# Performance work log

Hardware: AMD Instinct MI355X
Metric: run time of the kernel (lower is better)

Reference implementation:

```python
import jax, jax.numpy as jnp
import numpy as np

COMMITMENT_COST = 0.25
NUM_EMBEDDINGS = 1024
EMBEDDING_DIM = 512  # win_size(8) * num_pellets(64)


def setup_inputs() -> dict:
    key = jax.random.key(0)
    k1, k2 = jax.random.split(key)
    inputs = jax.random.normal(k1, (64, 256, EMBEDDING_DIM), dtype=jnp.float32)
    # matches torch init: uniform_(-1/K, 1/K)
    lim = 1.0 / NUM_EMBEDDINGS
    emb_weight = jax.random.uniform(k2, (NUM_EMBEDDINGS, EMBEDDING_DIM),
                                    dtype=jnp.float32, minval=-lim, maxval=lim)
    return {"inputs": inputs, "emb_weight": emb_weight}


def reference(inputs, emb_weight):
    batch_size = inputs.shape[0]
    input_shape = inputs.shape
    flat = inputs.reshape(-1, EMBEDDING_DIM)  # [N, D]

    distances = (jnp.sum(flat * flat, axis=1, keepdims=True)
                 + jnp.sum(emb_weight * emb_weight, axis=1)
                 - 2.0 * flat @ emb_weight.T)
    encoding_indices = jnp.argmin(distances, axis=1)  # [N]

    # gather instead of one-hot matmul (same math)
    quantized = emb_weight[encoding_indices].reshape(input_shape)

    e_latent_loss = jnp.mean((jax.lax.stop_gradient(quantized) - inputs) ** 2)
    q_latent_loss = jnp.mean((quantized - jax.lax.stop_gradient(inputs)) ** 2)
    loss_vq = q_latent_loss + COMMITMENT_COST * e_latent_loss

    # straight-through estimator
    quantized = inputs + jax.lax.stop_gradient(quantized - inputs)

    encoding_indices = encoding_indices.reshape(batch_size, -1)
    return loss_vq, quantized, encoding_indices
```

## Files before the change

kernel.cpp:

```cpp
#include <hip/hip_runtime.h>
#include <cfloat>

#define NROWS  16384
#define DIM    512
#define KC     1024
#define QELEMS (NROWS * DIM)

#define NSPLIT 8

typedef float  floatx4 __attribute__((ext_vector_type(4)));
typedef _Float16 half8 __attribute__((ext_vector_type(8)));
typedef _Float16 half4 __attribute__((ext_vector_type(4)));

__device__ __forceinline__ void gl_lds16(const _Float16* g, void* l) {
    __builtin_amdgcn_global_load_lds(
        (const __attribute__((address_space(1))) unsigned int*)g,
        (__attribute__((address_space(3))) unsigned int*)l,
        16, 0, 0);
}

__global__ __launch_bounds__(256) void prep_a_kernel(const float* __restrict__ A,
                                                     float* __restrict__ xsq,
                                                     _Float16* __restrict__ ah,
                                                     _Float16* __restrict__ al,
                                                     unsigned long long* __restrict__ packed,
                                                     float* __restrict__ out) {
    if (blockIdx.x == 0 && threadIdx.x == 0) out[0] = 0.f;
    int wave = threadIdx.x >> 6, lane = threadIdx.x & 63;
    int row = blockIdx.x * 4 + wave;
    const float4* Mr = (const float4*)(A + (size_t)row * DIM);
    float4 va = Mr[lane];
    float4 vb = Mr[lane + 64];
    float s = 0.f;
    s += va.x*va.x + va.y*va.y + va.z*va.z + va.w*va.w;
    s += vb.x*vb.x + vb.y*vb.y + vb.z*vb.z + vb.w*vb.w;
    #pragma unroll
    for (int off = 32; off; off >>= 1) s += __shfl_down(s, off, 64);
    if (lane == 0) { xsq[row] = s; packed[row] = ~0ULL; }

    float xa[4] = {va.x, va.y, va.z, va.w}, xb[4] = {vb.x, vb.y, vb.z, vb.w};
    half4 ha, la, hb, lb;
    #pragma unroll
    for (int e = 0; e < 4; ++e) {
        float t = xa[e] * 2048.0f;
        _Float16 h = (_Float16)t;
        ha[e] = h; la[e] = (_Float16)(t - (float)h);
        t = xb[e] * 2048.0f;
        h = (_Float16)t;
        hb[e] = h; lb[e] = (_Float16)(t - (float)h);
    }
    _Float16* ar = ah + (size_t)row * DIM;
    _Float16* lr = al + (size_t)row * DIM;
    ((half4*)ar)[lane]      = ha;
    ((half4*)lr)[lane]      = la;
    ((half4*)ar)[lane + 64] = hb;
    ((half4*)lr)[lane + 64] = lb;
}

__global__ __launch_bounds__(256) void prep_e_kernel(const float* __restrict__ E,
                                                     float* __restrict__ esq,
                                                     _Float16* __restrict__ eh,
                                                     _Float16* __restrict__ el) {
    int wave = threadIdx.x >> 6, lane = threadIdx.x & 63;
    int row = blockIdx.x * 4 + wave;
    const float4* Mr = (const float4*)(E + (size_t)row * DIM);
    float4 va = Mr[lane];
    float4 vb = Mr[lane + 64];
    float s = 0.f;
    s += va.x*va.x + va.y*va.y + va.z*va.z + va.w*va.w;
    s += vb.x*vb.x + vb.y*vb.y + vb.z*vb.z + vb.w*vb.w;
    #pragma unroll
    for (int off = 32; off; off >>= 1) s += __shfl_down(s, off, 64);
    if (lane == 0) esq[row] = s;

    float xa[4] = {va.x, va.y, va.z, va.w}, xb[4] = {vb.x, vb.y, vb.z, vb.w};
    half4 ha, la, hb, lb;
    #pragma unroll
    for (int e = 0; e < 4; ++e) {
        float t = xa[e] * 65536.0f;
        _Float16 h = (_Float16)t;
        ha[e] = h; la[e] = (_Float16)(t - (float)h);
        t = xb[e] * 65536.0f;
        h = (_Float16)t;
        hb[e] = h; lb[e] = (_Float16)(t - (float)h);
    }
    _Float16* hr = eh + (size_t)row * DIM;
    _Float16* lr = el + (size_t)row * DIM;
    ((half4*)hr)[lane]      = ha;
    ((half4*)lr)[lane]      = la;
    ((half4*)hr)[lane + 64] = hb;
    ((half4*)lr)[lane + 64] = lb;
}

__global__ __launch_bounds__(256) void mfma_argmin_kernel(const _Float16* __restrict__ ah,
                                                          const _Float16* __restrict__ al,
                                                          const _Float16* __restrict__ eh,
                                                          const _Float16* __restrict__ el,
                                                          const float* __restrict__ esq,
                                                          const float* __restrict__ xsq,
                                                          unsigned long long* __restrict__ packed) {
    __shared__ half8 AhT[512], AlT[512], EhT[512], ElT[512];
    __shared__ float redv[128][2];
    __shared__ int   redi[128][2];

    const int tid = threadIdx.x;
    const int lane = tid & 63, wave = tid >> 6;
    const int wm = wave >> 1, wn = wave & 1;
    const int tx = lane & 15, qd = lane >> 4;
    const int bm = blockIdx.x & 127, bn = blockIdx.x >> 7;
    const int m0 = bm * 128, c0 = bn * 128;

    const int rowL = (wave & 1) * 64 + lane;
    const int kqL  = wave >> 1;
    size_t offA = (size_t)(m0 + rowL) * DIM + kqL * 8;
    size_t offE = (size_t)(c0 + rowL) * DIM + kqL * 8;
    const int cb0 = wave * 64, cb1 = 256 + wave * 64;

    floatx4 acc[4][4];
    #pragma unroll
    for (int i = 0; i < 4; ++i)
        #pragma unroll
        for (int j = 0; j < 4; ++j) acc[i][j] = (floatx4){0.f, 0.f, 0.f, 0.f};

    #pragma unroll 1
    for (int kt = 0; kt < DIM / 32; ++kt) {
        gl_lds16(ah + offA,      &AhT[cb0]);
        gl_lds16(ah + offA + 16, &AhT[cb1]);
        gl_lds16(al + offA,      &AlT[cb0]);
        gl_lds16(al + offA + 16, &AlT[cb1]);
        gl_lds16(eh + offE,      &EhT[cb0]);
        gl_lds16(eh + offE + 16, &EhT[cb1]);
        gl_lds16(el + offE,      &ElT[cb0]);
        gl_lds16(el + offE + 16, &ElT[cb1]);
        offA += 32; offE += 32;
        __syncthreads();

        half8 fa[4], fbh[4], fbl[4];
        #pragma unroll
        for (int i = 0; i < 4; ++i)
            fa[i] = AhT[qd * 128 + wm * 64 + i * 16 + tx];
        #pragma unroll
        for (int j = 0; j < 4; ++j) {
            fbh[j] = EhT[qd * 128 + wn * 64 + j * 16 + tx];
            fbl[j] = ElT[qd * 128 + wn * 64 + j * 16 + tx];
        }
        #pragma unroll
        for (int i = 0; i < 4; ++i)
            #pragma unroll
            for (int j = 0; j < 4; ++j)
                acc[i][j] = __builtin_amdgcn_mfma_f32_16x16x32_f16(fa[i], fbh[j], acc[i][j], 0, 0, 0);
        #pragma unroll
        for (int i = 0; i < 4; ++i)
            #pragma unroll
            for (int j = 0; j < 4; ++j)
                acc[i][j] = __builtin_amdgcn_mfma_f32_16x16x32_f16(fa[i], fbl[j], acc[i][j], 0, 0, 0);
        #pragma unroll
        for (int i = 0; i < 4; ++i)
            fa[i] = AlT[qd * 128 + wm * 64 + i * 16 + tx];
        #pragma unroll
        for (int i = 0; i < 4; ++i)
            #pragma unroll
            for (int j = 0; j < 4; ++j)
                acc[i][j] = __builtin_amdgcn_mfma_f32_16x16x32_f16(fa[i], fbh[j], acc[i][j], 0, 0, 0);
        __syncthreads();
    }

    float sqe_v[4];
    #pragma unroll
    for (int j = 0; j < 4; ++j) sqe_v[j] = esq[c0 + wn * 64 + j * 16 + tx];
    #pragma unroll
    for (int i = 0; i < 4; ++i) {
        #pragma unroll
        for (int r = 0; r < 4; ++r) {
            int rl = wm * 64 + i * 16 + qd * 4 + r;
            float sx = xsq[m0 + rl];
            float bvv = FLT_MAX; int bii = 0x7fffffff;
            #pragma unroll
            for (int j = 0; j < 4; ++j) {
                float S = sx + sqe_v[j];
                float s = S - acc[i][j][r] * (1.0f / 67108864.0f);
                int c = c0 + wn * 64 + j * 16 + tx;
                if (s < bvv || (s == bvv && c < bii)) { bvv = s; bii = c; }
            }
            #pragma unroll
            for (int md = 1; md < 16; md <<= 1) {
                float ov = __shfl_xor(bvv, md, 64);
                int   oc = __shfl_xor(bii, md, 64);
                if (ov < bvv || (ov == bvv && oc < bii)) { bvv = ov; bii = oc; }
            }
            if (tx == 0) { redv[rl][wn] = bvv; redi[rl][wn] = bii; }
        }
    }
    __syncthreads();
    if (tid < 128) {
        float v0 = redv[tid][0], v1 = redv[tid][1];
        int   i0 = redi[tid][0], i1 = redi[tid][1];
        float v = (v1 < v0) ? v1 : v0;
        int   ix = (v1 < v0) ? i1 : i0;
        unsigned long long pk = ((unsigned long long)__float_as_uint(v) << 32)
                              | (unsigned int)ix;
        atomicMin(&packed[m0 + tid], pk);
    }
}

__global__ __launch_bounds__(256) void finalize_kernel(const float* __restrict__ A,
                                                       const float* __restrict__ E,
                                                       const unsigned long long* __restrict__ packed,
                                                       float* __restrict__ out) {
    float* q = out + 1;
    float* idxF = out + 1 + QELEMS;
    const int tid = threadIdx.x;
    const int r0 = blockIdx.x * 32;

    __shared__ int sidx[32];
    if (tid < 32) {
        int idx = (int)(unsigned int)(packed[r0 + tid] & 0xFFFFFFFFull);
        sidx[tid] = idx;
        idxF[r0 + tid] = (float)idx;
    }
    __syncthreads();

    float sacc = 0.f;
    #pragma unroll 4
    for (int it = 0; it < 16; ++it) {
        int flat = it * 256 + tid;
        int row = flat >> 7;
        int d4  = (flat & 127) * 4;
        int idx = sidx[row];
        float4 e = *(const float4*)(E + (size_t)idx * DIM + d4);
        float4 x = *(const float4*)(A + (size_t)(r0 + row) * DIM + d4);
        *(float4*)(q + (size_t)(r0 + row) * DIM + d4) = e;
        float d0 = e.x - x.x, d1 = e.y - x.y, d2 = e.z - x.z, d3 = e.w - x.w;
        sacc += d0*d0 + d1*d1 + d2*d2 + d3*d3;
    }
    #pragma unroll
    for (int off = 32; off; off >>= 1) sacc += __shfl_down(sacc, off, 64);
    __shared__ float ps[4];
    if ((tid & 63) == 0) ps[tid >> 6] = sacc;
    __syncthreads();
    if (tid == 0)
        atomicAdd(out, (ps[0] + ps[1] + ps[2] + ps[3]) * (1.25f / (float)QELEMS));
}

extern "C" void kernel_launch(void* const* d_in, const int* in_sizes, int n_in,
                              void* d_out, int out_size, void* d_ws, size_t ws_size,
                              hipStream_t stream) {
    const float* A = (const float*)d_in[0];
    const float* E = (const float*)d_in[1];
    float* out = (float*)d_out;

    unsigned long long* packed = (unsigned long long*)d_ws;
    float*    esq  = (float*)(packed + NROWS);
    float*    xsq  = esq + KC;
    _Float16* eh   = (_Float16*)(xsq + NROWS);
    _Float16* el   = eh + (size_t)KC * DIM;
    _Float16* ah   = el + (size_t)KC * DIM;
    _Float16* al   = ah + (size_t)NROWS * DIM;

    prep_a_kernel<<<NROWS / 4, 256, 0, stream>>>(A, xsq, ah, al, packed, out);
    prep_e_kernel<<<KC / 4,    256, 0, stream>>>(E, esq, eh, el);
    mfma_argmin_kernel<<<(NROWS / 128) * NSPLIT, 256, 0, stream>>>(
        ah, al, eh, el, esq, xsq, packed);
    finalize_kernel<<<NROWS / 32, 256, 0, stream>>>(A, E, packed, out);
}
```

Measured before the change: 190.8 us.

## Double-buffer LDS tiles in MFMA argmin loop and merge prep kernels

Merges the two input-preparation kernels into one launch that branches on block index to process either the input rows or the codebook rows. In the MFMA distance/argmin kernel, the shared-memory tiles become double-buffered: the next K-slice is issued with async global-to-LDS loads while the current slice is consumed, which removes one barrier per iteration. This aims to hide global load latency behind the MFMA work and to save one launch. In exchange LDS use doubles, which may lower occupancy, and correctness relies on the async LDS writes being visible after the single end-of-iteration barrier.

```diff
diff --git a/kernel.cpp b/kernel.cpp
--- a/kernel.cpp
+++ b/kernel.cpp
@@ -19,16 +19,24 @@
         16, 0, 0);
 }
 
-__global__ __launch_bounds__(256) void prep_a_kernel(const float* __restrict__ A,
-                                                     float* __restrict__ xsq,
-                                                     _Float16* __restrict__ ah,
-                                                     _Float16* __restrict__ al,
-                                                     unsigned long long* __restrict__ packed,
-                                                     float* __restrict__ out) {
+__global__ __launch_bounds__(256) void prep_kernel(const float* __restrict__ A,
+                                                   const float* __restrict__ E,
+                                                   float* __restrict__ xsq,
+                                                   float* __restrict__ esq,
+                                                   _Float16* __restrict__ ah,
+                                                   _Float16* __restrict__ al,
+                                                   _Float16* __restrict__ eh,
+                                                   _Float16* __restrict__ el,
+                                                   unsigned long long* __restrict__ packed,
+                                                   float* __restrict__ out) {
     if (blockIdx.x == 0 && threadIdx.x == 0) out[0] = 0.f;
-    int wave = threadIdx.x >> 6, lane = threadIdx.x & 63;
-    int row = blockIdx.x * 4 + wave;
-    const float4* Mr = (const float4*)(A + (size_t)row * DIM);
+    const int wave = threadIdx.x >> 6, lane = threadIdx.x & 63;
+    const bool isA = blockIdx.x < (NROWS / 4);
+    const int row = (isA ? blockIdx.x : blockIdx.x - NROWS / 4) * 4 + wave;
+    const float* M = isA ? A : E;
+    const float scale = isA ? 2048.0f : 65536.0f;
+
+    const float4* Mr = (const float4*)(M + (size_t)row * DIM);
     float4 va = Mr[lane];
     float4 vb = Mr[lane + 64];
     float s = 0.f;
@@ -36,56 +44,24 @@
     s += vb.x*vb.x + vb.y*vb.y + vb.z*vb.z + vb.w*vb.w;
     #pragma unroll
     for (int off = 32; off; off >>= 1) s += __shfl_down(s, off, 64);
-    if (lane == 0) { xsq[row] = s; packed[row] = ~0ULL; }
+    if (lane == 0) {
+        if (isA) { xsq[row] = s; packed[row] = ~0ULL; }
+        else     { esq[row] = s; }
+    }
 
     float xa[4] = {va.x, va.y, va.z, va.w}, xb[4] = {vb.x, vb.y, vb.z, vb.w};
     half4 ha, la, hb, lb;
     #pragma unroll
     for (int e = 0; e < 4; ++e) {
-        float t = xa[e] * 2048.0f;
+        float t = xa[e] * scale;
         _Float16 h = (_Float16)t;
         ha[e] = h; la[e] = (_Float16)(t - (float)h);
-        t = xb[e] * 2048.0f;
+        t = xb[e] * scale;
         h = (_Float16)t;
         hb[e] = h; lb[e] = (_Float16)(t - (float)h);
     }
-    _Float16* ar = ah + (size_t)row * DIM;
-    _Float16* lr = al + (size_t)row * DIM;
-    ((half4*)ar)[lane]      = ha;
-    ((half4*)lr)[lane]      = la;
-    ((half4*)ar)[lane + 64] = hb;
-    ((half4*)lr)[lane + 64] = lb;
-}
-
-__global__ __launch_bounds__(256) void prep_e_kernel(const float* __restrict__ E,
-                                                     float* __restrict__ esq,
-                                                     _Float16* __restrict__ eh,
-                                                     _Float16* __restrict__ el) {
-    int wave = threadIdx.x >> 6, lane = threadIdx.x & 63;
-    int row = blockIdx.x * 4 + wave;
-    const float4* Mr = (const float4*)(E + (size_t)row * DIM);
-    float4 va = Mr[lane];
-    float4 vb = Mr[lane + 64];
-    float s = 0.f;
-    s += va.x*va.x + va.y*va.y + va.z*va.z + va.w*va.w;
-    s += vb.x*vb.x + vb.y*vb.y + vb.z*vb.z + vb.w*vb.w;
-    #pragma unroll
-    for (int off = 32; off; off >>= 1) s += __shfl_down(s, off, 64);
-    if (lane == 0) esq[row] = s;
-
-    float xa[4] = {va.x, va.y, va.z, va.w}, xb[4] = {vb.x, vb.y, vb.z, vb.w};
-    half4 ha, la, hb, lb;
-    #pragma unroll
-    for (int e = 0; e < 4; ++e) {
-        float t = xa[e] * 65536.0f;
-        _Float16 h = (_Float16)t;
-        ha[e] = h; la[e] = (_Float16)(t - (float)h);
-        t = xb[e] * 65536.0f;
-        h = (_Float16)t;
-        hb[e] = h; lb[e] = (_Float16)(t - (float)h);
-    }
-    _Float16* hr = eh + (size_t)row * DIM;
-    _Float16* lr = el + (size_t)row * DIM;
+    _Float16* hr = (isA ? ah : eh) + (size_t)row * DIM;
+    _Float16* lr = (isA ? al : el) + (size_t)row * DIM;
     ((half4*)hr)[lane]      = ha;
     ((half4*)lr)[lane]      = la;
     ((half4*)hr)[lane + 64] = hb;
@@ -99,7 +75,7 @@
                                                           const float* __restrict__ esq,
                                                           const float* __restrict__ xsq,
                                                           unsigned long long* __restrict__ packed) {
-    __shared__ half8 AhT[512], AlT[512], EhT[512], ElT[512];
+    __shared__ half8 AhT[2][512], AlT[2][512], EhT[2][512], ElT[2][512];
     __shared__ float redv[128][2];
     __shared__ int   redi[128][2];
 
@@ -122,27 +98,40 @@
         #pragma unroll
         for (int j = 0; j < 4; ++j) acc[i][j] = (floatx4){0.f, 0.f, 0.f, 0.f};
 
+    gl_lds16(ah + offA,      &AhT[0][cb0]);
+    gl_lds16(ah + offA + 16, &AhT[0][cb1]);
+    gl_lds16(al + offA,      &AlT[0][cb0]);
+    gl_lds16(al + offA + 16, &AlT[0][cb1]);
+    gl_lds16(eh + offE,      &EhT[0][cb0]);
+    gl_lds16(eh + offE + 16, &EhT[0][cb1]);
+    gl_lds16(el + offE,      &ElT[0][cb0]);
+    gl_lds16(el + offE + 16, &ElT[0][cb1]);
+    offA += 32; offE += 32;
+    __syncthreads();
+
     #pragma unroll 1
     for (int kt = 0; kt < DIM / 32; ++kt) {
-        gl_lds16(ah + offA,      &AhT[cb0]);
-        gl_lds16(ah + offA + 16, &AhT[cb1]);
-        gl_lds16(al + offA,      &AlT[cb0]);
-        gl_lds16(al + offA + 16, &AlT[cb1]);
-        gl_lds16(eh + offE,      &EhT[cb0]);
-        gl_lds16(eh + offE + 16, &EhT[cb1]);
-        gl_lds16(el + offE,      &ElT[cb0]);
-        gl_lds16(el + offE + 16, &ElT[cb1]);
-        offA += 32; offE += 32;
-        __syncthreads();
+        const int cur = kt & 1, nxt = cur ^ 1;
+        if (kt < DIM / 32 - 1) {
+            gl_lds16(ah + offA,      &AhT[nxt][cb0]);
+            gl_lds16(ah + offA + 16, &AhT[nxt][cb1]);
+            gl_lds16(al + offA,      &AlT[nxt][cb0]);
+            gl_lds16(al + offA + 16, &AlT[nxt][cb1]);
+            gl_lds16(eh + offE,      &EhT[nxt][cb0]);
+            gl_lds16(eh + offE + 16, &EhT[nxt][cb1]);
+            gl_lds16(el + offE,      &ElT[nxt][cb0]);
+            gl_lds16(el + offE + 16, &ElT[nxt][cb1]);
+            offA += 32; offE += 32;
+        }
 
         half8 fa[4], fbh[4], fbl[4];
         #pragma unroll
         for (int i = 0; i < 4; ++i)
-            fa[i] = AhT[qd * 128 + wm * 64 + i * 16 + tx];
+            fa[i] = AhT[cur][qd * 128 + wm * 64 + i * 16 + tx];
         #pragma unroll
         for (int j = 0; j < 4; ++j) {
-            fbh[j] = EhT[qd * 128 + wn * 64 + j * 16 + tx];
-            fbl[j] = ElT[qd * 128 + wn * 64 + j * 16 + tx];
+            fbh[j] = EhT[cur][qd * 128 + wn * 64 + j * 16 + tx];
+            fbl[j] = ElT[cur][qd * 128 + wn * 64 + j * 16 + tx];
         }
         #pragma unroll
         for (int i = 0; i < 4; ++i)
@@ -156,12 +145,13 @@
                 acc[i][j] = __builtin_amdgcn_mfma_f32_16x16x32_f16(fa[i], fbl[j], acc[i][j], 0, 0, 0);
         #pragma unroll
         for (int i = 0; i < 4; ++i)
-            fa[i] = AlT[qd * 128 + wm * 64 + i * 16 + tx];
+            fa[i] = AlT[cur][qd * 128 + wm * 64 + i * 16 + tx];
         #pragma unroll
         for (int i = 0; i < 4; ++i)
             #pragma unroll
             for (int j = 0; j < 4; ++j)
                 acc[i][j] = __builtin_amdgcn_mfma_f32_16x16x32_f16(fa[i], fbh[j], acc[i][j], 0, 0, 0);
+
         __syncthreads();
     }
 
@@ -257,8 +247,7 @@
     _Float16* ah   = el + (size_t)KC * DIM;
     _Float16* al   = ah + (size_t)NROWS * DIM;
 
-    prep_a_kernel<<<NROWS / 4, 256, 0, stream>>>(A, xsq, ah, al, packed, out);
-    prep_e_kernel<<<KC / 4,    256, 0, stream>>>(E, esq, eh, el);
+    prep_kernel<<<NROWS / 4 + KC / 4, 256, 0, stream>>>(A, E, xsq, esq, ah, al, eh, el, packed, out);
     mfma_argmin_kernel<<<(NROWS / 128) * NSPLIT, 256, 0, stream>>>(
         ah, al, eh, el, esq, xsq, packed);
     finalize_kernel<<<NROWS / 32, 256, 0, stream>>>(A, E, packed, out);
```

Result: no change. 191.6 us (+0.4%).
